# Kernel optimization log

Hardware: AMD Instinct MI355X
Metric: run time of the kernel (lower is better)

Reference implementation:

```python
import jax, jax.numpy as jnp
import numpy as np
from jax import lax

EPS = 1e-5
K = 16  # MixedOp.self.k


def conv(x, w, stride=1, pad=0, dil=1, groups=1):
    return lax.conv_general_dilated(
        x, w, (stride, stride), [(pad, pad), (pad, pad)],
        rhs_dilation=(dil, dil), feature_group_count=groups,
        dimension_numbers=('NCHW', 'OIHW', 'NCHW'))


def bn(x):
    # BatchNorm2d(affine=False) in training mode: normalize with batch stats
    m = jnp.mean(x, axis=(0, 2, 3), keepdims=True)
    v = jnp.var(x, axis=(0, 2, 3), keepdims=True)
    return (x - m) * lax.rsqrt(v + EPS)


def maxpool3(x):
    return lax.reduce_window(x, -jnp.inf, lax.max, (1, 1, 3, 3), (1, 1, 1, 1),
                             [(0, 0), (0, 0), (1, 1), (1, 1)])


def avgpool3(x):
    # AvgPool2d(3, stride=1, padding=1, count_include_pad=False)
    s = lax.reduce_window(x, 0., lax.add, (1, 1, 3, 3), (1, 1, 1, 1),
                          [(0, 0), (0, 0), (1, 1), (1, 1)])
    c = lax.reduce_window(jnp.ones_like(x), 0., lax.add, (1, 1, 3, 3),
                          (1, 1, 1, 1), [(0, 0), (0, 0), (1, 1), (1, 1)])
    return s / c


def sep_conv(x, dw1, pw1, dw2, pw2):
    C = x.shape[1]
    p = dw1.shape[-1] // 2
    h = jax.nn.relu(x)
    h = conv(h, dw1, pad=p, groups=C)
    h = bn(conv(h, pw1))
    h = jax.nn.relu(h)
    h = conv(h, dw2, pad=p, groups=C)
    return bn(conv(h, pw2))


def dil_conv(x, dw, pw):
    C = x.shape[1]
    p = (dw.shape[-1] // 2) * 2  # dilation=2 padding (3x3->2, 5x5->4)
    h = jax.nn.relu(x)
    h = conv(h, dw, pad=p, dil=2, groups=C)
    return bn(conv(h, pw))


def setup_inputs() -> dict:
    key = jax.random.key(0)
    C, B, H, W = 256, 32, 64, 64
    c_op = C // K  # 16 channels fed to each candidate op
    ks = jax.random.split(key, 17)
    g = lambda k, shp, fan: jax.random.normal(k, shp, jnp.float32) / np.sqrt(fan)
    return {
        'x': jax.random.normal(ks[0], (B, C, H, W), jnp.float32),
        # ChannelAttention se: 1x1 convs, reduction=2
        'ca_w1': g(ks[1], (C // 2, C, 1, 1), C),
        'ca_w2': g(ks[2], (C, C // 2, 1, 1), C // 2),
        # sep_conv_3x3 (two dw+pw stages)
        's3_dw1': g(ks[3], (c_op, 1, 3, 3), 9),
        's3_pw1': g(ks[4], (c_op, c_op, 1, 1), c_op),
        's3_dw2': g(ks[5], (c_op, 1, 3, 3), 9),
        's3_pw2': g(ks[6], (c_op, c_op, 1, 1), c_op),
        # sep_conv_5x5
        's5_dw1': g(ks[7], (c_op, 1, 5, 5), 25),
        's5_pw1': g(ks[8], (c_op, c_op, 1, 1), c_op),
        's5_dw2': g(ks[9], (c_op, 1, 5, 5), 25),
        's5_pw2': g(ks[10], (c_op, c_op, 1, 1), c_op),
        # dil_conv_3x3 / dil_conv_5x5
        'd3_dw': g(ks[11], (c_op, 1, 3, 3), 9),
        'd3_pw': g(ks[12], (c_op, c_op, 1, 1), c_op),
        'd5_dw': g(ks[13], (c_op, 1, 5, 5), 25),
        'd5_pw': g(ks[14], (c_op, c_op, 1, 1), c_op),
        # AttentionModule fc: channel = 8*c_op = 128, ratio = 8
        'at_w1': g(ks[15], (c_op, 8 * c_op), 8 * c_op),  # Linear(128->16)
        'at_w2': g(ks[16], (8 * c_op, c_op), c_op),      # Linear(16->128)
    }


def reference(x, ca_w1, ca_w2, s3_dw1, s3_pw1, s3_dw2, s3_pw2,
              s5_dw1, s5_pw1, s5_dw2, s5_pw2, d3_dw, d3_pw, d5_dw, d5_pw,
              at_w1, at_w2):
    B, C, H, W = x.shape
    c_sel = C // K  # number of selected channels (16)

    # ---- ChannelAttention ----
    mx = jnp.max(x, axis=(2, 3), keepdims=True)   # [B,C,1,1]
    av = jnp.mean(x, axis=(2, 3), keepdims=True)
    se = lambda z: conv(jax.nn.relu(conv(z, ca_w1)), ca_w2)
    num_list = jax.nn.sigmoid(se(mx) + se(av))    # [B,C,1,1]

    aux = x                                       # auxiliary_op = Identity (stride=1)
    xg = x * num_list

    # ---- top-k channel routing ----
    slist = jnp.sum(num_list, axis=0).reshape(C)  # sum over batch
    _, idx = lax.top_k(slist, c_sel)              # sorted, largest first
    xt = xg[:, idx]                               # gather [B,c_sel,H,W]

    # ---- 8 candidate branches (DARTS PRIMITIVES, stride=1) ----
    branches = [
        jnp.zeros_like(xt),                       # none
        bn(maxpool3(xt)),                         # max_pool_3x3 + BN
        bn(avgpool3(xt)),                         # avg_pool_3x3 + BN
        xt,                                       # skip_connect (Identity)
        sep_conv(xt, s3_dw1, s3_pw1, s3_dw2, s3_pw2),
        sep_conv(xt, s5_dw1, s5_pw1, s5_dw2, s5_pw2),
        dil_conv(xt, d3_dw, d3_pw),
        dil_conv(xt, d5_dw, d5_pw),
    ]
    temp = jnp.concatenate(branches, axis=1)      # [B, 8*c_sel, H, W]

    # ---- AttentionModule ----
    y = jnp.mean(temp, axis=(2, 3))               # [B, 8*c_sel]
    y = jax.nn.sigmoid(jax.nn.relu(y @ at_w1.T) @ at_w2.T)
    att = temp * y[:, :, None, None]
    op_attention = jnp.sum(y.reshape(B, 8, c_sel), axis=(0, 2))  # [8]

    # sum the 8 branch chunks
    out = jnp.sum(att.reshape(B, 8, c_sel, H, W), axis=1)

    # scatter back into gated x, then residual add
    xg = xg.at[:, idx].set(out)
    return xg + aux, op_attention
```

## Files before the change

### kernel.cpp

```cpp
#include <hip/hip_runtime.h>
#include <math.h>

static constexpr int B = 32, C = 256, HW = 4096, CS = 16;
static constexpr int BHW = B * HW;
static constexpr size_t IMG = (size_t)B * CS * HW;

static constexpr size_t OFF_S    = 0;
static constexpr size_t OFF_SQ   = 4096;
static constexpr size_t OFF_U    = 8192;
static constexpr size_t OFF_CNT  = 8256;
static constexpr size_t ACC_END  = 8260;
static constexpr size_t OFF_MX   = 8320;
static constexpr size_t OFF_AV   = OFF_MX + 8192;
static constexpr size_t OFF_NUM  = OFF_AV + 8192;
static constexpr size_t OFF_Y    = OFF_NUM + 8192;
static constexpr size_t OFF_ACO  = OFF_Y + 4096;
static constexpr size_t OFF_BIAS = OFF_ACO + 4096;
static constexpr size_t OFF_INT  = OFF_BIAS + 512;
static constexpr size_t OFF_R    = OFF_INT + 384;

__device__ inline float wave_sum(float v) {
  v += __shfl_down(v, 32); v += __shfl_down(v, 16); v += __shfl_down(v, 8);
  v += __shfl_down(v, 4);  v += __shfl_down(v, 2);  v += __shfl_down(v, 1);
  return v;
}
__device__ inline float wave_max(float v) {
  v = fmaxf(v, __shfl_down(v, 32)); v = fmaxf(v, __shfl_down(v, 16));
  v = fmaxf(v, __shfl_down(v, 8));  v = fmaxf(v, __shfl_down(v, 4));
  v = fmaxf(v, __shfl_down(v, 2));  v = fmaxf(v, __shfl_down(v, 1));
  return v;
}

__global__ __launch_bounds__(256) void k_stats(const float4* __restrict__ x,
                                               float* __restrict__ mx, float* __restrict__ av,
                                               float* __restrict__ accbase) {
  int bc = blockIdx.x;
  if (bc == 0) for (int i = threadIdx.x; i < (int)ACC_END; i += 256) accbase[i] = 0.f;
  const float4* p = x + (size_t)bc * 1024;
  float mmax = -INFINITY, msum = 0.f;
  for (int i = threadIdx.x; i < 1024; i += 256) {
    float4 v = p[i];
    mmax = fmaxf(mmax, fmaxf(fmaxf(v.x, v.y), fmaxf(v.z, v.w)));
    msum += v.x + v.y + v.z + v.w;
  }
  __shared__ float rs[4], rm[4];
  float s = wave_sum(msum), m = wave_max(mmax);
  int w = threadIdx.x >> 6;
  if ((threadIdx.x & 63) == 0) { rs[w] = s; rm[w] = m; }
  __syncthreads();
  if (threadIdx.x == 0) {
    mx[bc] = fmaxf(fmaxf(rm[0], rm[1]), fmaxf(rm[2], rm[3]));
    av[bc] = (rs[0] + rs[1] + rs[2] + rs[3]) * (1.f / 4096.f);
  }
}

__global__ __launch_bounds__(256) void k_sesel(const float* __restrict__ mx, const float* __restrict__ av,
                                               const float* __restrict__ w1, const float* __restrict__ w2,
                                               float* __restrict__ num,
                                               int* __restrict__ idx, int* __restrict__ selmap,
                                               unsigned* __restrict__ cnt) {
  __shared__ float zs0[256], zs1[256], h0[128], h1[128];
  __shared__ unsigned lastv;
  int b = blockIdx.x, t = threadIdx.x;
  zs0[t] = mx[b * 256 + t]; zs1[t] = av[b * 256 + t];
  __syncthreads();
  if (t < 128) {
    const float* wr = w1 + (size_t)t * 256;
    float am = 0.f, aa = 0.f;
    for (int i = 0; i < 256; i++) { float w = wr[i]; am = fmaf(w, zs0[i], am); aa = fmaf(w, zs1[i], aa); }
    h0[t] = fmaxf(am, 0.f); h1[t] = fmaxf(aa, 0.f);
  }
  __syncthreads();
  {
    const float* wr = w2 + (size_t)t * 128;
    float sm = 0.f, sa = 0.f;
    for (int j = 0; j < 128; j++) { float w = wr[j]; sm = fmaf(w, h0[j], sm); sa = fmaf(w, h1[j], sa); }
    num[b * 256 + t] = 1.f / (1.f + expf(-(sm + sa)));
  }
  __threadfence();
  if (t == 0) lastv = atomicAdd(cnt, 1u);
  __syncthreads();
  if (lastv == 31u) {
    __threadfence();
    float acc = 0.f;
    for (int bb = 0; bb < B; bb++) acc += num[bb * 256 + t];
    zs0[t] = acc; selmap[t] = -1;
    __syncthreads();
    float v = zs0[t];
    int rank = 0;
    for (int c = 0; c < 256; c++) {
      float o = zs0[c];
      rank += (o > v) || (o == v && c < t);
    }
    if (rank < 16) { idx[rank] = t; selmap[t] = rank; }
  }
}

__global__ __launch_bounds__(256) void k_fuseA(
    const float* __restrict__ x, const float* __restrict__ num, const int* __restrict__ idx,
    const float* __restrict__ d3dw, const float* __restrict__ d5dw,
    const float* __restrict__ s3dw1, const float* __restrict__ s5dw1,
    float* __restrict__ R, float* __restrict__ scr,
    float* __restrict__ S, float* __restrict__ SQ) {
  __shared__ float lt[24 * 72];
  __shared__ float red[20];
  const int t = threadIdx.x;
  const int blk = blockIdx.x;
  const int bk = blk >> 2, qt = blk & 3;
  const int b = bk >> 4, k = bk & 15;
  const int c = idx[k];
  const float sc = num[b * 256 + c];
  const float* src = x + ((size_t)b * 256 + c) * HW;
  const size_t o = (size_t)bk * HW + qt * 1024;
  const int ry0 = qt * 16;
  for (int i = t; i < 24 * 72; i += 256) {
    int ty = i / 72, tx = i - ty * 72;
    int y = ry0 - 4 + ty, xx = tx - 4;
    float v = 0.f;
    if ((unsigned)y < 64u && (unsigned)xx < 64u) v = src[y * 64 + xx] * sc;
    lt[i] = v;
  }
  __syncthreads();
  {
    float s1 = 0.f, q1 = 0.f, s2 = 0.f, q2 = 0.f, s3 = 0.f;
    for (int i = t; i < 1024; i += 256) {
      int lr = i >> 6, col = i & 63;
      int y = ry0 + lr;
      const float* ctr = lt + (lr + 4) * 72 + (col + 4);
      int dy0 = (y > 0) ? -1 : 0, dy1 = (y < 63) ? 1 : 0;
      int dx0 = (col > 0) ? -1 : 0, dx1 = (col < 63) ? 1 : 0;
      float mxv = -INFINITY, sm = 0.f;
      for (int dy = dy0; dy <= dy1; dy++)
        for (int dx = dx0; dx <= dx1; dx++) { float v = ctr[dy * 72 + dx]; mxv = fmaxf(mxv, v); sm += v; }
      float avv = sm / (float)((dy1 - dy0 + 1) * (dx1 - dx0 + 1));
      R[o + i] = mxv; R[IMG + o + i] = avv;
      s1 += mxv; q1 += mxv * mxv; s2 += avv; q2 += avv * avv; s3 += ctr[0];
    }
    s1 = wave_sum(s1); q1 = wave_sum(q1); s2 = wave_sum(s2); q2 = wave_sum(q2); s3 = wave_sum(s3);
    int w = t >> 6;
    if ((t & 63) == 0) { red[w] = s1; red[4 + w] = q1; red[8 + w] = s2; red[12 + w] = q2; red[16 + w] = s3; }
    __syncthreads();
    if (t == 0) {
      atomicAdd(&S[512 + bk],   red[0] + red[1] + red[2] + red[3]);
      atomicAdd(&SQ[512 + bk],  red[4] + red[5] + red[6] + red[7]);
      atomicAdd(&S[1024 + bk],  red[8] + red[9] + red[10] + red[11]);
      atomicAdd(&SQ[1024 + bk], red[12] + red[13] + red[14] + red[15]);
      atomicAdd(&S[1536 + bk],  red[16] + red[17] + red[18] + red[19]);
    }
  }
  {
    float w[9];
#pragma unroll
    for (int i = 0; i < 9; i++) w[i] = d3dw[k * 9 + i];
    for (int i = t; i < 1024; i += 256) {
      int lr = i >> 6, col = i & 63;
      const float* ctr = lt + (lr + 4) * 72 + (col + 4);
      float acc = 0.f;
#pragma unroll
      for (int a = 0; a < 3; a++)
#pragma unroll
        for (int q = 0; q < 3; q++)
          acc = fmaf(w[a * 3 + q], fmaxf(ctr[(2 * a - 2) * 72 + (2 * q - 2)], 0.f), acc);
      scr[0 * IMG + o + i] = acc;
    }
  }
  {
    float w[25];
#pragma unroll
    for (int i = 0; i < 25; i++) w[i] = d5dw[k * 25 + i];
    for (int i = t; i < 1024; i += 256) {
      int lr = i >> 6, col = i & 63;
      const float* ctr = lt + (lr + 4) * 72 + (col + 4);
      float acc = 0.f;
#pragma unroll
      for (int a = 0; a < 5; a++)
#pragma unroll
        for (int q = 0; q < 5; q++)
          acc = fmaf(w[a * 5 + q], fmaxf(ctr[(2 * a - 4) * 72 + (2 * q - 4)], 0.f), acc);
      scr[1 * IMG + o + i] = acc;
    }
  }
  {
    float w[9];
#pragma unroll
    for (int i = 0; i < 9; i++) w[i] = s3dw1[k * 9 + i];
    for (int i = t; i < 1024; i += 256) {
      int lr = i >> 6, col = i & 63;
      const float* ctr = lt + (lr + 4) * 72 + (col + 4);
      float acc = 0.f;
#pragma unroll
      for (int a = 0; a < 3; a++)
#pragma unroll
        for (int q = 0; q < 3; q++)
          acc = fmaf(w[a * 3 + q], fmaxf(ctr[(a - 1) * 72 + (q - 1)], 0.f), acc);
      scr[2 * IMG + o + i] = acc;
    }
  }
  {
    float w[25];
#pragma unroll
    for (int i = 0; i < 25; i++) w[i] = s5dw1[k * 25 + i];
    for (int i = t; i < 1024; i += 256) {
      int lr = i >> 6, col = i & 63;
      const float* ctr = lt + (lr + 4) * 72 + (col + 4);
      float acc = 0.f;
#pragma unroll
      for (int a = 0; a < 5; a++)
#pragma unroll
        for (int q = 0; q < 5; q++)
          acc = fmaf(w[a * 5 + q], fmaxf(ctr[(a - 2) * 72 + (q - 2)], 0.f), acc);
      scr[3 * IMG + o + i] = acc;
    }
  }
}

__device__ __forceinline__ void pw4(const float* __restrict__ in, const float* __restrict__ w16,
                                    float* __restrict__ out, float* __restrict__ sacc,
                                    float* __restrict__ qacc, int perB, int b, int q4,
                                    float* wsh, float* redS, float* redQ) {
  int t = threadIdx.x;
  wsh[t] = w16[t];
  size_t base = (size_t)b * 16 * HW + q4 * 1024 + t * 4;
  float4 sv[16];
#pragma unroll
  for (int i = 0; i < 16; i++) sv[i] = *(const float4*)(in + base + (size_t)i * HW);
  __syncthreads();
  int wv = t >> 6, lane = t & 63;
#pragma unroll
  for (int cc = 0; cc < 16; cc++) {
    float4 o; o.x = 0.f; o.y = 0.f; o.z = 0.f; o.w = 0.f;
#pragma unroll
    for (int i = 0; i < 16; i++) {
      float w = wsh[cc * 16 + i];
      o.x = fmaf(w, sv[i].x, o.x); o.y = fmaf(w, sv[i].y, o.y);
      o.z = fmaf(w, sv[i].z, o.z); o.w = fmaf(w, sv[i].w, o.w);
    }
    *(float4*)(out + base + (size_t)cc * HW) = o;
    float s = (o.x + o.y) + (o.z + o.w);
    float qv = fmaf(o.x, o.x, fmaf(o.y, o.y, fmaf(o.z, o.z, o.w * o.w)));
    s = wave_sum(s); qv = wave_sum(qv);
    if (lane == 0) { redS[cc * 4 + wv] = s; redQ[cc * 4 + wv] = qv; }
  }
  __syncthreads();
  if (t < 16) {
    float s = redS[t * 4] + redS[t * 4 + 1] + redS[t * 4 + 2] + redS[t * 4 + 3];
    float q = redQ[t * 4] + redQ[t * 4 + 1] + redQ[t * 4 + 2] + redQ[t * 4 + 3];
    int sl = perB ? b * 16 + t : t;
    atomicAdd(&sacc[sl], s); atomicAdd(&qacc[sl], q);
  }
}

__global__ __launch_bounds__(256) void k_fuseB(
    const float* __restrict__ scr,
    const float* __restrict__ d3pw, const float* __restrict__ d5pw,
    const float* __restrict__ s3pw1, const float* __restrict__ s5pw1,
    float* __restrict__ R, float* __restrict__ t3, float* __restrict__ t5,
    float* __restrict__ S, float* __restrict__ SQ, float* __restrict__ U) {
  __shared__ float wsh[256], redS[64], redQ[64];
  int blk = blockIdx.x;
  int op = blk >> 7, rem = blk & 127;
  int b = rem >> 2, q4 = rem & 3;
  switch (op) {
    case 0: pw4(scr + 0 * IMG, d3pw,  R + 4 * IMG, S + 6 * 512, SQ + 6 * 512, 1, b, q4, wsh, redS, redQ); break;
    case 1: pw4(scr + 1 * IMG, d5pw,  R + 5 * IMG, S + 7 * 512, SQ + 7 * 512, 1, b, q4, wsh, redS, redQ); break;
    case 2: pw4(scr + 2 * IMG, s3pw1, t3, U + 0,  U + 16, 0, b, q4, wsh, redS, redQ); break;
    case 3: pw4(scr + 3 * IMG, s5pw1, t5, U + 32, U + 48, 0, b, q4, wsh, redS, redQ); break;
  }
}

template<int KK>
__device__ __forceinline__ void dw_q(const float* __restrict__ src, const float* __restrict__ w,
                                     float* __restrict__ dst, float* lt, float mu, float rs, int qt) {
  constexpr int P = KK / 2, TW = 64 + 2 * P, ROWS = 16 + 2 * P;
  float wr[KK * KK];
#pragma unroll
  for (int i = 0; i < KK * KK; i++) wr[i] = w[i];
  const int t = threadIdx.x;
  const int ry0 = qt * 16;
  for (int i = t; i < ROWS * TW; i += 256) {
    int ty = i / TW, tx = i - ty * TW;
    int y = ry0 - P + ty, xx = tx - P;
    float v = 0.f;
    if ((unsigned)y < 64u && (unsigned)xx < 64u) {
      v = src[y * 64 + xx];
      v = (v - mu) * rs;
      v = fmaxf(v, 0.f);
    }
    lt[i] = v;
  }
  __syncthreads();
  for (int i = t; i < 1024; i += 256) {
    int lr = i >> 6, col = i & 63;
    const float* t0 = lt + lr * TW + col;
    float acc = 0.f;
#pragma unroll
    for (int a = 0; a < KK; a++)
#pragma unroll
      for (int q = 0; q < KK; q++)
        acc = fmaf(wr[a * KK + q], t0[a * TW + q], acc);
    dst[qt * 1024 + i] = acc;
  }
}

__global__ __launch_bounds__(256) void k_fuseC(
    const float* __restrict__ t3, const float* __restrict__ t5,
    const float* __restrict__ s3dw2, const float* __restrict__ s5dw2,
    float* __restrict__ scr, const float* __restrict__ U) {
  __shared__ float lt[20 * 68];
  int blk = blockIdx.x;
  int op = blk >> 11, rem = blk & 2047;
  int bk = rem >> 2, qt = rem & 3, k = bk & 15;
  size_t o = (size_t)bk * HW;
  if (op == 0) {
    float mu = U[k] * (1.f / (float)BHW);
    float var = U[16 + k] * (1.f / (float)BHW) - mu * mu;
    dw_q<3>(t3 + o, s3dw2 + k * 9, scr + 0 * IMG + o, lt, mu, rsqrtf(var + 1e-5f), qt);
  } else {
    float mu = U[32 + k] * (1.f / (float)BHW);
    float var = U[48 + k] * (1.f / (float)BHW) - mu * mu;
    dw_q<5>(t5 + o, s5dw2 + k * 25, scr + 1 * IMG + o, lt, mu, rsqrtf(var + 1e-5f), qt);
  }
}

__global__ __launch_bounds__(256) void k_fuseD(
    const float* __restrict__ scr,
    const float* __restrict__ s3pw2, const float* __restrict__ s5pw2,
    float* __restrict__ R, float* __restrict__ S, float* __restrict__ SQ) {
  __shared__ float wsh[256], redS[64], redQ[64];
  int blk = blockIdx.x;
  int op = blk >> 7, rem = blk & 127;
  int b = rem >> 2, q4 = rem & 3;
  if (op == 0) pw4(scr + 0 * IMG, s3pw2, R + 2 * IMG, S + 4 * 512, SQ + 4 * 512, 1, b, q4, wsh, redS, redQ);
  else         pw4(scr + 1 * IMG, s5pw2, R + 3 * IMG, S + 5 * 512, SQ + 5 * 512, 1, b, q4, wsh, redS, redQ);
}

__global__ __launch_bounds__(128) void k_att(const float* __restrict__ S, const float* __restrict__ SQ,
                                             const float* __restrict__ w1, const float* __restrict__ w2,
                                             float* __restrict__ y, float* __restrict__ aco,
                                             float* __restrict__ bia) {
  int b = blockIdx.x, t = threadIdx.x;
  __shared__ float ym[128], h[16], msh[8][16], rssh[8][16], ysh[128];
  int op = t >> 4, k = t & 15;
  bool isbn = (op == 1 || op == 2 || op >= 4);
  float m = 0.f, rsc = 0.f;
  {
    float ss = 0.f, qq = 0.f;
    for (int bb = 0; bb < B; bb++) { ss += S[op * 512 + bb * 16 + k]; qq += SQ[op * 512 + bb * 16 + k]; }
    if (isbn) {
      m = ss * (1.f / (float)BHW);
      float var = qq * (1.f / (float)BHW) - m * m;
      rsc = rsqrtf(var + 1e-5f);
    }
  }
  msh[op][k] = m; rssh[op][k] = rsc;
  float sm = S[op * 512 + b * 16 + k] * (1.f / 4096.f);
  float yme = (op == 0) ? 0.f : ((op == 3) ? sm : (sm - m) * rsc);
  ym[t] = yme;
  __syncthreads();
  if (t < 16) {
    const float* wr = w1 + (size_t)t * 128;
    float acc = 0.f;
    for (int c = 0; c < 128; c++) acc = fmaf(wr[c], ym[c], acc);
    h[t] = fmaxf(acc, 0.f);
  }
  __syncthreads();
  {
    const float* wr = w2 + (size_t)t * 16;
    float acc = 0.f;
    for (int j = 0; j < 16; j++) acc = fmaf(wr[j], h[j], acc);
    float yy = 1.f / (1.f + expf(-acc));
    ysh[t] = yy; y[b * 128 + t] = yy;
  }
  __syncthreads();
  if (t < 16) {
    float bias = 0.f;
    for (int o2 = 1; o2 < 8; o2++) {
      float yv = ysh[o2 * 16 + t];
      float a;
      if (o2 == 3) a = yv;
      else { a = yv * rssh[o2][t]; bias -= yv * rssh[o2][t] * msh[o2][t]; }
      aco[(b * 16 + t) * 8 + o2] = a;
    }
    bia[b * 16 + t] = bias;
  }
}

__global__ __launch_bounds__(256) void k_final(const float* __restrict__ x, const float* __restrict__ num,
                                               const int* __restrict__ selmap, const int* __restrict__ idx,
                                               const float* __restrict__ rbuf, const float* __restrict__ aco,
                                               const float* __restrict__ bia, const float* __restrict__ ybuf,
                                               float* __restrict__ out, float* __restrict__ out8) {
  __shared__ float sh[256];
  int bc = blockIdx.x;
  if (bc == B * C) {
    int t = threadIdx.x, op = t >> 5, lane = t & 31;
    float acc = 0.f;
    for (int i = lane; i < 512; i += 32) { int bb = i >> 4, kk = i & 15; acc += ybuf[bb * 128 + op * 16 + kk]; }
    sh[t] = acc;
    __syncthreads();
    if (lane == 0) {
      float s = 0.f;
      for (int i = 0; i < 32; i++) s += sh[op * 32 + i];
      out8[op] = s;
    }
    return;
  }
  int b = bc >> 8;
  int k = selmap[bc & 255];
  const float4* xs = (const float4*)(x + (size_t)bc * HW);
  float4* od = (float4*)(out + (size_t)bc * HW);
  if (k < 0) {
    float sc = 1.f + num[bc];
    for (int i = threadIdx.x; i < 1024; i += 256) {
      float4 v = xs[i];
      v.x *= sc; v.y *= sc; v.z *= sc; v.w *= sc;
      od[i] = v;
    }
  } else {
    int bk = b * 16 + k;
    int ci = idx[k];
    float scn = num[b * 256 + ci];
    const float4* xtp = (const float4*)(x + ((size_t)b * 256 + ci) * HW);
    const float4* r0 = (const float4*)(rbuf + ((size_t)0 * 512 + bk) * HW);
    const float4* r1 = (const float4*)(rbuf + ((size_t)1 * 512 + bk) * HW);
    const float4* r2 = (const float4*)(rbuf + ((size_t)2 * 512 + bk) * HW);
    const float4* r3 = (const float4*)(rbuf + ((size_t)3 * 512 + bk) * HW);
    const float4* r4 = (const float4*)(rbuf + ((size_t)4 * 512 + bk) * HW);
    const float4* r5 = (const float4*)(rbuf + ((size_t)5 * 512 + bk) * HW);
    float a1 = aco[bk * 8 + 1], a2 = aco[bk * 8 + 2], a3 = aco[bk * 8 + 3] * scn, a4 = aco[bk * 8 + 4];
    float a5 = aco[bk * 8 + 5], a6 = aco[bk * 8 + 6], a7 = aco[bk * 8 + 7];
    float bias = bia[bk];
    for (int i = threadIdx.x; i < 1024; i += 256) {
      float4 xv = xs[i], tv = xtp[i];
      float4 v0 = r0[i], v1 = r1[i], v2 = r2[i], v3 = r3[i], v4 = r4[i], v5 = r5[i];
      float4 o;
      o.x = xv.x + bias + a1 * v0.x + a2 * v1.x + a3 * tv.x + a4 * v2.x + a5 * v3.x + a6 * v4.x + a7 * v5.x;
      o.y = xv.y + bias + a1 * v0.y + a2 * v1.y + a3 * tv.y + a4 * v2.y + a5 * v3.y + a6 * v4.y + a7 * v5.y;
      o.z = xv.z + bias + a1 * v0.z + a2 * v1.z + a3 * tv.z + a4 * v2.z + a5 * v3.z + a6 * v4.z + a7 * v5.z;
      o.w = xv.w + bias + a1 * v0.w + a2 * v1.w + a3 * tv.w + a4 * v2.w + a5 * v3.w + a6 * v4.w + a7 * v5.w;
      od[i] = o;
    }
  }
}

extern "C" void kernel_launch(void* const* d_in, const int* in_sizes, int n_in,
                              void* d_out, int out_size, void* d_ws, size_t ws_size,
                              hipStream_t stream) {
  const float* x      = (const float*)d_in[0];
  const float* ca_w1  = (const float*)d_in[1];
  const float* ca_w2  = (const float*)d_in[2];
  const float* s3_dw1 = (const float*)d_in[3];
  const float* s3_pw1 = (const float*)d_in[4];
  const float* s3_dw2 = (const float*)d_in[5];
  const float* s3_pw2 = (const float*)d_in[6];
  const float* s5_dw1 = (const float*)d_in[7];
  const float* s5_pw1 = (const float*)d_in[8];
  const float* s5_dw2 = (const float*)d_in[9];
  const float* s5_pw2 = (const float*)d_in[10];
  const float* d3_dw  = (const float*)d_in[11];
  const float* d3_pw  = (const float*)d_in[12];
  const float* d5_dw  = (const float*)d_in[13];
  const float* d5_pw  = (const float*)d_in[14];
  const float* at_w1  = (const float*)d_in[15];
  const float* at_w2  = (const float*)d_in[16];

  float* ws = (float*)d_ws;
  float* S = ws + OFF_S;  float* SQ = ws + OFF_SQ;  float* U = ws + OFF_U;
  unsigned* cnt = (unsigned*)(ws + OFF_CNT);
  float* mx = ws + OFF_MX; float* av = ws + OFF_AV; float* num = ws + OFF_NUM;
  float* ybuf = ws + OFF_Y; float* aco = ws + OFF_ACO; float* bia = ws + OFF_BIAS;
  int* ib = (int*)(ws + OFF_INT);
  int* idx = ib; int* selmap = ib + 16;
  float* R = ws + OFF_R;

  float* outf = (float*)d_out;
  float* scr = outf;
  float* t3  = outf + 4 * IMG;
  float* t5  = outf + 5 * IMG;
  float* out8 = outf + (size_t)B * C * HW;

  k_stats<<<B * C, 256, 0, stream>>>((const float4*)x, mx, av, ws);
  k_sesel<<<B, 256, 0, stream>>>(mx, av, ca_w1, ca_w2, num, idx, selmap, cnt);
  k_fuseA<<<2048, 256, 0, stream>>>(x, num, idx, d3_dw, d5_dw, s3_dw1, s5_dw1, R, scr, S, SQ);
  k_fuseB<<<512, 256, 0, stream>>>(scr, d3_pw, d5_pw, s3_pw1, s5_pw1, R, t3, t5, S, SQ, U);
  k_fuseC<<<4096, 256, 0, stream>>>(t3, t5, s3_dw2, s5_dw2, scr, U);
  k_fuseD<<<256, 256, 0, stream>>>(scr, s3_pw2, s5_pw2, R, S, SQ);
  k_att<<<B, 128, 0, stream>>>(S, SQ, at_w1, at_w2, ybuf, aco, bia);
  k_final<<<B * C + 1, 256, 0, stream>>>(x, num, selmap, idx, R, aco, bia, ybuf, outf, out8);
}
```

Before: 199.9 us.

## Recompute pooling branches in final kernel and fold attention into fuseD tail

The max and avg pool outputs are no longer written to global memory in k_fuseA. k_final now recomputes them from a shared-memory copy of the scaled input channel, which also serves as the skip branch. The separate k_att launch is removed: the last k_fuseD block, found with an atomic counter plus threadfences, computes the attention MLP for all batches. This trades redundant pooling arithmetic and a serial tail block for less global traffic and one fewer launch; the counter at cnt+1 must be zeroed each call.

```diff
diff --git a/kernel.cpp b/kernel.cpp
--- a/kernel.cpp
+++ b/kernel.cpp
@@ -100,8 +100,7 @@
     const float* __restrict__ x, const float* __restrict__ num, const int* __restrict__ idx,
     const float* __restrict__ d3dw, const float* __restrict__ d5dw,
     const float* __restrict__ s3dw1, const float* __restrict__ s5dw1,
-    float* __restrict__ R, float* __restrict__ scr,
-    float* __restrict__ S, float* __restrict__ SQ) {
+    float* __restrict__ scr, float* __restrict__ S, float* __restrict__ SQ) {
   __shared__ float lt[24 * 72];
   __shared__ float red[20];
   const int t = threadIdx.x;
@@ -133,7 +132,6 @@
       for (int dy = dy0; dy <= dy1; dy++)
         for (int dx = dx0; dx <= dx1; dx++) { float v = ctr[dy * 72 + dx]; mxv = fmaxf(mxv, v); sm += v; }
       float avv = sm / (float)((dy1 - dy0 + 1) * (dx1 - dx0 + 1));
-      R[o + i] = mxv; R[IMG + o + i] = avv;
       s1 += mxv; q1 += mxv * mxv; s2 += avv; q2 += avv * avv; s3 += ctr[0];
     }
     s1 = wave_sum(s1); q1 = wave_sum(q1); s2 = wave_sum(s2); q2 = wave_sum(q2); s3 = wave_sum(s3);
@@ -325,72 +323,83 @@
 __global__ __launch_bounds__(256) void k_fuseD(
     const float* __restrict__ scr,
     const float* __restrict__ s3pw2, const float* __restrict__ s5pw2,
-    float* __restrict__ R, float* __restrict__ S, float* __restrict__ SQ) {
+    float* __restrict__ R, float* __restrict__ S, float* __restrict__ SQ,
+    const float* __restrict__ w1, const float* __restrict__ w2,
+    float* __restrict__ ybuf, float* __restrict__ aco, float* __restrict__ bia,
+    unsigned* __restrict__ cnt) {
   __shared__ float wsh[256], redS[64], redQ[64];
+  __shared__ unsigned lastv;
   int blk = blockIdx.x;
   int op = blk >> 7, rem = blk & 127;
   int b = rem >> 2, q4 = rem & 3;
   if (op == 0) pw4(scr + 0 * IMG, s3pw2, R + 2 * IMG, S + 4 * 512, SQ + 4 * 512, 1, b, q4, wsh, redS, redQ);
   else         pw4(scr + 1 * IMG, s5pw2, R + 3 * IMG, S + 5 * 512, SQ + 5 * 512, 1, b, q4, wsh, redS, redQ);
-}
-
-__global__ __launch_bounds__(128) void k_att(const float* __restrict__ S, const float* __restrict__ SQ,
-                                             const float* __restrict__ w1, const float* __restrict__ w2,
-                                             float* __restrict__ y, float* __restrict__ aco,
-                                             float* __restrict__ bia) {
-  int b = blockIdx.x, t = threadIdx.x;
-  __shared__ float ym[128], h[16], msh[8][16], rssh[8][16], ysh[128];
-  int op = t >> 4, k = t & 15;
-  bool isbn = (op == 1 || op == 2 || op >= 4);
-  float m = 0.f, rsc = 0.f;
-  {
+  int t = threadIdx.x;
+  __threadfence();
+  __syncthreads();
+  if (t == 0) lastv = atomicAdd(cnt, 1u);
+  __syncthreads();
+  if (lastv != 255u) return;
+  __threadfence();
+  __shared__ float msh[128], rssh[128], ym2[16][129], hh2[16][17], ysh2[16][129];
+  if (t < 128) {
+    int op2 = t >> 4, k = t & 15;
+    bool isbn = (op2 == 1 || op2 == 2 || op2 >= 4);
     float ss = 0.f, qq = 0.f;
-    for (int bb = 0; bb < B; bb++) { ss += S[op * 512 + bb * 16 + k]; qq += SQ[op * 512 + bb * 16 + k]; }
-    if (isbn) {
-      m = ss * (1.f / (float)BHW);
-      float var = qq * (1.f / (float)BHW) - m * m;
-      rsc = rsqrtf(var + 1e-5f);
-    }
-  }
-  msh[op][k] = m; rssh[op][k] = rsc;
-  float sm = S[op * 512 + b * 16 + k] * (1.f / 4096.f);
-  float yme = (op == 0) ? 0.f : ((op == 3) ? sm : (sm - m) * rsc);
-  ym[t] = yme;
-  __syncthreads();
-  if (t < 16) {
-    const float* wr = w1 + (size_t)t * 128;
-    float acc = 0.f;
-    for (int c = 0; c < 128; c++) acc = fmaf(wr[c], ym[c], acc);
-    h[t] = fmaxf(acc, 0.f);
-  }
-  __syncthreads();
-  {
-    const float* wr = w2 + (size_t)t * 16;
-    float acc = 0.f;
-    for (int j = 0; j < 16; j++) acc = fmaf(wr[j], h[j], acc);
-    float yy = 1.f / (1.f + expf(-acc));
-    ysh[t] = yy; y[b * 128 + t] = yy;
-  }
-  __syncthreads();
-  if (t < 16) {
-    float bias = 0.f;
-    for (int o2 = 1; o2 < 8; o2++) {
-      float yv = ysh[o2 * 16 + t];
-      float a;
-      if (o2 == 3) a = yv;
-      else { a = yv * rssh[o2][t]; bias -= yv * rssh[o2][t] * msh[o2][t]; }
-      aco[(b * 16 + t) * 8 + o2] = a;
-    }
-    bia[b * 16 + t] = bias;
+    for (int bb = 0; bb < B; bb++) { ss += S[op2 * 512 + bb * 16 + k]; qq += SQ[op2 * 512 + bb * 16 + k]; }
+    float m = 0.f, rsc = 0.f;
+    if (isbn) { m = ss * (1.f / (float)BHW); float var = qq * (1.f / (float)BHW) - m * m; rsc = rsqrtf(var + 1e-5f); }
+    msh[t] = m; rssh[t] = rsc;
+  }
+  __syncthreads();
+  for (int half = 0; half < 2; half++) {
+    int b0 = half * 16;
+    for (int e = t; e < 2048; e += 256) {
+      int bb = e >> 7, cc = e & 127, op2 = cc >> 4;
+      float sm = S[op2 * 512 + (b0 + bb) * 16 + (cc & 15)] * (1.f / 4096.f);
+      ym2[bb][cc] = (op2 == 0) ? 0.f : ((op2 == 3) ? sm : (sm - msh[cc]) * rssh[cc]);
+    }
+    __syncthreads();
+    {
+      int bb = t >> 4, u = t & 15;
+      const float* wr = w1 + (size_t)u * 128;
+      float acc = 0.f;
+      for (int c2 = 0; c2 < 128; c2++) acc = fmaf(wr[c2], ym2[bb][c2], acc);
+      hh2[bb][u] = fmaxf(acc, 0.f);
+    }
+    __syncthreads();
+    for (int e = t; e < 2048; e += 256) {
+      int bb = e >> 7, oo = e & 127;
+      const float* wr = w2 + (size_t)oo * 16;
+      float acc = 0.f;
+      for (int j = 0; j < 16; j++) acc = fmaf(wr[j], hh2[bb][j], acc);
+      float yy = 1.f / (1.f + expf(-acc));
+      ysh2[bb][oo] = yy; ybuf[(b0 + bb) * 128 + oo] = yy;
+    }
+    __syncthreads();
+    {
+      int bb = t >> 4, kk = t & 15;
+      float bias = 0.f;
+      for (int o2 = 1; o2 < 8; o2++) {
+        float yv = ysh2[bb][o2 * 16 + kk];
+        float a;
+        if (o2 == 3) a = yv;
+        else { a = yv * rssh[o2 * 16 + kk]; bias -= a * msh[o2 * 16 + kk]; }
+        aco[((b0 + bb) * 16 + kk) * 8 + o2] = a;
+      }
+      bia[(b0 + bb) * 16 + kk] = bias;
+    }
+    __syncthreads();
   }
 }
 
 __global__ __launch_bounds__(256) void k_final(const float* __restrict__ x, const float* __restrict__ num,
-                                               const int* __restrict__ selmap, const int* __restrict__ idx,
+                                               const int* __restrict__ selmap,
                                                const float* __restrict__ rbuf, const float* __restrict__ aco,
                                                const float* __restrict__ bia, const float* __restrict__ ybuf,
                                                float* __restrict__ out, float* __restrict__ out8) {
   __shared__ float sh[256];
+  __shared__ float lt[4096];
   int bc = blockIdx.x;
   if (bc == B * C) {
     int t = threadIdx.x, op = t >> 5, lane = t & 31;
@@ -407,9 +416,9 @@
   }
   int b = bc >> 8;
   int k = selmap[bc & 255];
-  const float4* xs = (const float4*)(x + (size_t)bc * HW);
-  float4* od = (float4*)(out + (size_t)bc * HW);
   if (k < 0) {
+    const float4* xs = (const float4*)(x + (size_t)bc * HW);
+    float4* od = (float4*)(out + (size_t)bc * HW);
     float sc = 1.f + num[bc];
     for (int i = threadIdx.x; i < 1024; i += 256) {
       float4 v = xs[i];
@@ -418,27 +427,28 @@
     }
   } else {
     int bk = b * 16 + k;
-    int ci = idx[k];
-    float scn = num[b * 256 + ci];
-    const float4* xtp = (const float4*)(x + ((size_t)b * 256 + ci) * HW);
-    const float4* r0 = (const float4*)(rbuf + ((size_t)0 * 512 + bk) * HW);
-    const float4* r1 = (const float4*)(rbuf + ((size_t)1 * 512 + bk) * HW);
-    const float4* r2 = (const float4*)(rbuf + ((size_t)2 * 512 + bk) * HW);
-    const float4* r3 = (const float4*)(rbuf + ((size_t)3 * 512 + bk) * HW);
-    const float4* r4 = (const float4*)(rbuf + ((size_t)4 * 512 + bk) * HW);
-    const float4* r5 = (const float4*)(rbuf + ((size_t)5 * 512 + bk) * HW);
-    float a1 = aco[bk * 8 + 1], a2 = aco[bk * 8 + 2], a3 = aco[bk * 8 + 3] * scn, a4 = aco[bk * 8 + 4];
-    float a5 = aco[bk * 8 + 5], a6 = aco[bk * 8 + 6], a7 = aco[bk * 8 + 7];
+    float scn = num[bc];
+    const float* xsc = x + (size_t)bc * HW;
+    float* odc = out + (size_t)bc * HW;
+    const float* r2 = rbuf + ((size_t)2 * 512 + bk) * HW;
+    const float* r3 = rbuf + ((size_t)3 * 512 + bk) * HW;
+    const float* r4 = rbuf + ((size_t)4 * 512 + bk) * HW;
+    const float* r5 = rbuf + ((size_t)5 * 512 + bk) * HW;
+    float a1 = aco[bk * 8 + 1], a2 = aco[bk * 8 + 2], a3 = aco[bk * 8 + 3];
+    float a4 = aco[bk * 8 + 4], a5 = aco[bk * 8 + 5], a6 = aco[bk * 8 + 6], a7 = aco[bk * 8 + 7];
     float bias = bia[bk];
-    for (int i = threadIdx.x; i < 1024; i += 256) {
-      float4 xv = xs[i], tv = xtp[i];
-      float4 v0 = r0[i], v1 = r1[i], v2 = r2[i], v3 = r3[i], v4 = r4[i], v5 = r5[i];
-      float4 o;
-      o.x = xv.x + bias + a1 * v0.x + a2 * v1.x + a3 * tv.x + a4 * v2.x + a5 * v3.x + a6 * v4.x + a7 * v5.x;
-      o.y = xv.y + bias + a1 * v0.y + a2 * v1.y + a3 * tv.y + a4 * v2.y + a5 * v3.y + a6 * v4.y + a7 * v5.y;
-      o.z = xv.z + bias + a1 * v0.z + a2 * v1.z + a3 * tv.z + a4 * v2.z + a5 * v3.z + a6 * v4.z + a7 * v5.z;
-      o.w = xv.w + bias + a1 * v0.w + a2 * v1.w + a3 * tv.w + a4 * v2.w + a5 * v3.w + a6 * v4.w + a7 * v5.w;
-      od[i] = o;
+    for (int p = threadIdx.x; p < HW; p += 256) lt[p] = xsc[p] * scn;
+    __syncthreads();
+    for (int p = threadIdx.x; p < HW; p += 256) {
+      int y = p >> 6, cx = p & 63;
+      int y0 = max(y - 1, 0), y1 = min(y + 1, 63), x0 = max(cx - 1, 0), x1 = min(cx + 1, 63);
+      float mxv = -INFINITY, sm = 0.f;
+      for (int yy = y0; yy <= y1; yy++)
+        for (int xx = x0; xx <= x1; xx++) { float v = lt[yy * 64 + xx]; mxv = fmaxf(mxv, v); sm += v; }
+      float avp = sm / (float)((y1 - y0 + 1) * (x1 - x0 + 1));
+      float g = lt[p];
+      odc[p] = xsc[p] + bias + a1 * mxv + a2 * avp + a3 * g
+             + a4 * r2[p] + a5 * r3[p] + a6 * r4[p] + a7 * r5[p];
     }
   }
 }
@@ -481,10 +491,9 @@
 
   k_stats<<<B * C, 256, 0, stream>>>((const float4*)x, mx, av, ws);
   k_sesel<<<B, 256, 0, stream>>>(mx, av, ca_w1, ca_w2, num, idx, selmap, cnt);
-  k_fuseA<<<2048, 256, 0, stream>>>(x, num, idx, d3_dw, d5_dw, s3_dw1, s5_dw1, R, scr, S, SQ);
+  k_fuseA<<<2048, 256, 0, stream>>>(x, num, idx, d3_dw, d5_dw, s3_dw1, s5_dw1, scr, S, SQ);
   k_fuseB<<<512, 256, 0, stream>>>(scr, d3_pw, d5_pw, s3_pw1, s5_pw1, R, t3, t5, S, SQ, U);
   k_fuseC<<<4096, 256, 0, stream>>>(t3, t5, s3_dw2, s5_dw2, scr, U);
-  k_fuseD<<<256, 256, 0, stream>>>(scr, s3_pw2, s5_pw2, R, S, SQ);
-  k_att<<<B, 128, 0, stream>>>(S, SQ, at_w1, at_w2, ybuf, aco, bia);
-  k_final<<<B * C + 1, 256, 0, stream>>>(x, num, selmap, idx, R, aco, bia, ybuf, outf, out8);
-}
+  k_fuseD<<<256, 256, 0, stream>>>(scr, s3_pw2, s5_pw2, R, S, SQ, at_w1, at_w2, ybuf, aco, bia, cnt + 1);
+  k_final<<<B * C + 1, 256, 0, stream>>>(x, num, selmap, R, aco, bia, ybuf, outf, out8);
+}
```

Measured after the change: 238.4 us. +19.3%, slower.
